# Optimization experiments

Measured on AMD Instinct MI355X. Metric: run time of the kernel, lower is better.

Reference implementation:

```python
import jax, jax.numpy as jnp
import numpy as np

N_LINKS = 10000
N_PATHS = 100000
LSD = 32   # link_state_dim
PSD = 32   # path_state_dim
T = 4
MAX_LEN = 12
RU = 256   # readout_units
OUT = 2


def _glorot(key, shape):
    return jax.random.normal(key, shape) * jnp.sqrt(2.0 / (shape[0] + shape[-1]))


def setup_inputs() -> dict:
    key = jax.random.key(0)
    ks = jax.random.split(key, 12)
    # variable path lengths 4..12 (mean 8)
    lengths = 4 + (np.arange(N_PATHS) % 9)
    E = int(lengths.sum())
    offsets = np.cumsum(lengths) - lengths
    paths = np.repeat(np.arange(N_PATHS), lengths)
    seqs = np.arange(E) - np.repeat(offsets, lengths)  # position of hop within its path
    rng = np.random.default_rng(0)
    links = rng.integers(0, N_LINKS, size=E)
    return {
        "capacities": jax.random.uniform(ks[0], (N_LINKS,), minval=1.0, maxval=10.0),
        "traffic": jax.random.uniform(ks[1], (N_PATHS,), minval=0.1, maxval=1.0),
        "links": jnp.asarray(links, jnp.int32),
        "paths": jnp.asarray(paths, jnp.int32),
        "seqs": jnp.asarray(seqs, jnp.int32),
        "n_links": N_LINKS,
        "n_paths": N_PATHS,
        "K_link": _glorot(ks[2], (LSD, 3 * LSD)),
        "R_link": _glorot(ks[3], (LSD, 3 * LSD)),
        "b_link": jnp.zeros((2, 3 * LSD)),
        "K_path": _glorot(ks[4], (LSD, 3 * PSD)),
        "R_path": _glorot(ks[5], (PSD, 3 * PSD)),
        "b_path": jnp.zeros((2, 3 * PSD)),
        "W1": _glorot(ks[6], (PSD, RU)),
        "b1": jnp.zeros((RU,)),
        "W2": _glorot(ks[7], (RU, RU)),
        "b2": jnp.zeros((RU,)),
        "Wf": _glorot(ks[8], (RU + PSD, OUT)),
        "bf": jnp.zeros((OUT,)),
    }


def _gru(x, h, K, R, b):
    # keras GRUCell, reset_after=True: separate input/recurrent biases
    xz = x @ K + b[0]
    hz = h @ R + b[1]
    xi_z, xi_r, xi_h = jnp.split(xz, 3, axis=-1)
    hi_z, hi_r, hi_h = jnp.split(hz, 3, axis=-1)
    z = jax.nn.sigmoid(xi_z + hi_z)
    r = jax.nn.sigmoid(xi_r + hi_r)
    hh = jnp.tanh(xi_h + r * hi_h)
    return z * h + (1.0 - z) * hh


def reference(capacities, traffic, links, paths, seqs, n_links, n_paths,
              K_link, R_link, b_link, K_path, R_path, b_path,
              W1, b1, W2, b2, Wf, bf):
    link_state = jnp.concatenate([capacities[:, None], jnp.zeros((n_links, LSD - 1))], axis=1)
    path_state = jnp.concatenate([traffic[:, None], jnp.zeros((n_paths, PSD - 1))], axis=1)

    lens = jax.ops.segment_sum(jnp.ones_like(paths), paths, num_segments=n_paths)  # [P]
    mask_t = (jnp.arange(MAX_LEN)[:, None] < lens[None, :])  # [L, P]

    for _ in range(T):
        h_ = link_state[links]  # gather: [E, LSD]
        # scatter into padded per-path sequences: [P, L, LSD]
        padded = jnp.zeros((n_paths, MAX_LEN, LSD), link_state.dtype).at[paths, seqs].set(h_)

        def step(h, xm):
            x_t, m_t = xm  # [P, LSD], [P]
            h_new = _gru(x_t, h, K_path, R_path, b_path)
            h = jnp.where(m_t[:, None], h_new, h)  # masked steps keep state
            return h, h

        path_state, outputs = jax.lax.scan(step, path_state, (padded.transpose(1, 0, 2), mask_t))
        m = outputs[seqs, paths]  # gather_nd: [E, PSD]
        m = jax.ops.segment_sum(m, links, num_segments=n_links)  # [n_links, PSD]
        link_state = _gru(m, link_state, K_link, R_link, b_link)

    h1 = jax.nn.selu(path_state @ W1 + b1)
    h2 = jax.nn.selu(h1 @ W2 + b2)
    pred = jnp.concatenate([h2, path_state], axis=1) @ Wf + bf
    return pred
```

## Files before the change

### kernel.cpp

```cpp
#include <hip/hip_runtime.h>
#include <hip/hip_bf16.h>

#define NPATHS 100000
#define NLINKS 10000
#define NEDGES 799996
#define TITERS 4
#define GRP    695

typedef __hip_bfloat16 bf16;
typedef unsigned short u16;
typedef unsigned int   u32;
typedef _Float16 half8 __attribute__((ext_vector_type(8)));
typedef __attribute__((ext_vector_type(4))) float float4v;

#define U_LNK 64
#define U_KPB 320064
#define U_RPB 323136
#define U_KLB 326208
#define U_RLB 329280
#define U_W1T 332352
#define U_W2T 340544
#define F_BP  203040
#define F_BL  203232
#define F_B1  203424
#define F_B2  203680
#define F_WF  203936
#define F_MAC 204544
#define F_PS  524544
#define B_ROWPTR 8498432u
#define B_SLOT   8538496u
#define B_CNT    11738496u
#define B_BUF    11778560u
#define CSR_WS_MIN 63000000ull

__device__ __forceinline__ float bf2f(bf16 v) { return __bfloat162float(v); }
__device__ __forceinline__ u16 f2h_u(float f) {
    _Float16 h = (_Float16)f; u16 u; __builtin_memcpy(&u, &h, 2); return u;
}
__device__ __forceinline__ float h2f_u(u16 u) {
    _Float16 h; __builtin_memcpy(&h, &u, 2); return (float)h;
}
__device__ __forceinline__ float loadf(const void* p, int i, int isbf) {
    return isbf ? bf2f(((const bf16*)p)[i]) : ((const float*)p)[i];
}
__device__ __forceinline__ float sigmoid_(float v) { return 1.f / (1.f + __expf(-v)); }
__device__ __forceinline__ float tanh_(float v) { return 1.f - 2.f / (__expf(2.f * v) + 1.f); }
__device__ __forceinline__ float selu_(float v) {
    return v > 0.f ? 1.0507009873554805f * v : 1.7580993408473766f * (__expf(v) - 1.f);
}
__device__ __forceinline__ u16* ps_row(u16* ps0, u16* ps1, u16* ps2, int p) {
    return p < 49999 ? ps0 + (size_t)p * 32
         : (p < 99998 ? ps1 + (size_t)(p - 49999) * 32
                      : ps2 + (size_t)(p - 99998) * 32);
}

__global__ void probe_kernel(const u32* __restrict__ cap, int* __restrict__ flag) {
    if (threadIdx.x == 0 && blockIdx.x == 0) {
        bool ok = true;
        for (int i = 0; i < 8; ++i) {
            u32 w = cap[i];
            u32 e1 = (w >> 7) & 0xFF, e2 = (w >> 23) & 0xFF;
            ok = ok && e1 >= 122 && e1 <= 133 && e2 >= 122 && e2 <= 133;
        }
        *flag = ok ? 1 : 0;
    }
}

__global__ __launch_bounds__(256) void init_kernel(
    const void* __restrict__ traf, const void* __restrict__ cap, const int* __restrict__ flag,
    float* __restrict__ wsf, u16* __restrict__ wsu, u16* ps0, u16* ps1, u16* ps2,
    const void* Kp, const void* Rp, const void* bp,
    const void* Kl, const void* Rl, const void* bl,
    const void* W1, const void* b1, const void* W2, const void* b2,
    const void* Wf, const void* bfv)
{
    const int isbf = *flag;
    const int i = blockIdx.x * 256 + threadIdx.x;
    if (i < NPATHS) {
        u32 ww[16];
        ww[0] = (u32)f2h_u(loadf(traf, i, isbf));
#pragma unroll
        for (int k = 1; k < 16; ++k) ww[k] = 0;
        uint4* row = (uint4*)ps_row(ps0, ps1, ps2, i);
        row[0] = *(uint4*)(ww + 0);  row[1] = *(uint4*)(ww + 4);
        row[2] = *(uint4*)(ww + 8);  row[3] = *(uint4*)(ww + 12);
    }
    int j;
    j = i;          if (j >= 0 && j < 320000)
        wsu[U_LNK + j] = ((j & 31) == 0) ? f2h_u(loadf(cap, j >> 5, isbf)) : (u16)0;
    j = i - 320000; if (j >= 0 && j < 3072) {
        int t = j >> 9, lane = (j >> 3) & 63, e = j & 7;
        int k = (lane >> 4) * 8 + e, n = t * 16 + (lane & 15);
        wsu[U_KPB + j] = f2h_u(loadf(Kp, k * 96 + n, isbf));
    }
    j = i - 323072; if (j >= 0 && j < 3072) {
        int t = j >> 9, lane = (j >> 3) & 63, e = j & 7;
        int k = (lane >> 4) * 8 + e, n = t * 16 + (lane & 15);
        wsu[U_RPB + j] = f2h_u(loadf(Rp, k * 96 + n, isbf));
    }
    j = i - 326144; if (j >= 0 && j < 3072) {
        int t = j >> 9, lane = (j >> 3) & 63, e = j & 7;
        int k = (lane >> 4) * 8 + e, n = t * 16 + (lane & 15);
        wsu[U_KLB + j] = f2h_u(loadf(Kl, k * 96 + n, isbf));
    }
    j = i - 329216; if (j >= 0 && j < 3072) {
        int t = j >> 9, lane = (j >> 3) & 63, e = j & 7;
        int k = (lane >> 4) * 8 + e, n = t * 16 + (lane & 15);
        wsu[U_RLB + j] = f2h_u(loadf(Rl, k * 96 + n, isbf));
    }
    j = i - 332288; if (j >= 0 && j < 192)   wsf[F_BP + j] = loadf(bp, j, isbf);
    j = i - 332480; if (j >= 0 && j < 192)   wsf[F_BL + j] = loadf(bl, j, isbf);
    j = i - 332672; if (j >= 0 && j < 256)   wsf[F_B1 + j] = loadf(b1, j, isbf);
    j = i - 332928; if (j >= 0 && j < 256)   wsf[F_B2 + j] = loadf(b2, j, isbf);
    j = i - 333184; if (j >= 0 && j < 578)
        wsf[F_WF + j] = (j < 576) ? loadf(Wf, j, isbf) : loadf(bfv, j - 576, isbf);
    j = i - 334000; if (j >= 0 && j < 8192) {
        int t = j >> 9, lane = (j >> 3) & 63, e = j & 7;
        int k = (lane >> 4) * 8 + e, n = t * 16 + (lane & 15);
        wsu[U_W1T + j] = f2h_u(loadf(W1, k * 256 + n, isbf));
    }
    j = i - 343000; if (j >= 0 && j < 65536) {
        int g = j >> 9, t = g >> 3, kb = g & 7;
        int lane = (j >> 3) & 63, e = j & 7;
        int k = kb * 32 + (lane >> 4) * 8 + e, n = t * 16 + (lane & 15);
        wsu[U_W2T + j] = f2h_u(loadf(W2, k * 256 + n, isbf));
    }
}

__global__ __launch_bounds__(256) void csr_count(const int* __restrict__ links,
                                                 int* __restrict__ cnt, int* __restrict__ slot) {
    int e = blockIdx.x * 256 + threadIdx.x;
    if (e < NEDGES) slot[e] = atomicAdd(&cnt[links[e]], 1);
}

__global__ __launch_bounds__(256) void csr_scan(const int* __restrict__ cnt,
                                                int* __restrict__ rowptr) {
    __shared__ int sd[256];
    __shared__ int sbase;
    const int tid = threadIdx.x;
    if (tid == 0) sbase = 0;
    __syncthreads();
    for (int chunk = 0; chunk < 40; ++chunk) {
        const int i = chunk * 256 + tid;
        const int v = (i < NLINKS) ? cnt[i] : 0;
        sd[tid] = v;
        __syncthreads();
        for (int off = 1; off < 256; off <<= 1) {
            int t = (tid >= off) ? sd[tid - off] : 0;
            __syncthreads();
            sd[tid] += t;
            __syncthreads();
        }
        if (i < NLINKS) rowptr[i] = sbase + sd[tid] - v;
        int ctot = sd[255];
        __syncthreads();
        if (tid == 0) sbase += ctot;
        __syncthreads();
    }
    if (tid == 0) rowptr[NLINKS] = sbase;
}

__global__ __launch_bounds__(256) void csr_slotadd(const int* __restrict__ links,
                                                   const int* __restrict__ rowptr,
                                                   int* __restrict__ slot) {
    int e = blockIdx.x * 256 + threadIdx.x;
    if (e < NEDGES) slot[e] += rowptr[links[e]];
}

__global__ __launch_bounds__(256, 3) void path_gru_mfma(
    const int* __restrict__ links,
    const u16* __restrict__ KPB, const u16* __restrict__ RPB,
    const float* __restrict__ bp,
    const u16* __restrict__ lnk16,
    u16* ps0, u16* ps1, u16* ps2, float* __restrict__ m_acc,
    const int* __restrict__ slot, u16* __restrict__ buf, const int csr)
{
    __shared__ u16 hlds[4][16 * 40];
    const int tid = threadIdx.x;
    const int wv = tid >> 6, lane = tid & 63;
    const int q = lane >> 4, col = lane & 15;
    const int w = blockIdx.x * 4 + wv;
    if (w >= 9 * GRP) return;
    const int c = w % 9;
    const int gi = w / 9;
    const int cnt = (c == 0) ? 11112 : 11111;
    const int idx0 = gi * 16;
    const int L = 4 + c;

    const int idxc = idx0 + col;
    const int actc = idxc < cnt;
    const int idcl = min(idxc, cnt - 1);
    const int pc   = c + 9 * idcl;
    const int offc = 4 * pc + idcl * 36 + (c * (c - 1)) / 2;

    u16* hw = hlds[wv];

    half8 KB[6], RB[6];
#pragma unroll
    for (int t = 0; t < 6; ++t) {
        KB[t] = *(const half8*)(KPB + t * 512 + lane * 8);
        RB[t] = *(const half8*)(RPB + t * 512 + lane * 8);
    }
    float xzb[6], hzb[6];
#pragma unroll
    for (int t = 0; t < 6; ++t) { xzb[t] = bp[t * 16 + col]; hzb[t] = bp[96 + t * 16 + col]; }

    half8 Ah = *(const half8*)(ps_row(ps0, ps1, ps2, pc) + q * 8);
    float hold[2][4];
#pragma unroll
    for (int t = 0; t < 2; ++t)
#pragma unroll
        for (int r = 0; r < 4; ++r) {
            int idr = min(idx0 + q * 4 + r, cnt - 1);
            int pr = c + 9 * idr;
            hold[t][r] = h2f_u(ps_row(ps0, ps1, ps2, pr)[t * 16 + col]);
        }

    int ln = actc ? links[offc] : -1;
    int sv = (csr && actc) ? slot[offc] : -1;
    half8 Ax = *(const half8*)(lnk16 + (size_t)max(ln, 0) * 32 + q * 8);

    for (int s = 0; s < L; ++s) {
        const int more = (s + 1 < L) && actc;
        const int ln_nxt = more ? links[offc + s + 1] : -1;
        const int sv_nxt = (csr && more) ? slot[offc + s + 1] : -1;
        const half8 Ax_nxt = *(const half8*)(lnk16 + (size_t)max(ln_nxt, 0) * 32 + q * 8);

        float4v xz[6], hz[6];
#pragma unroll
        for (int t = 0; t < 6; ++t) {
            float4v ix = {xzb[t], xzb[t], xzb[t], xzb[t]};
            float4v ih = {hzb[t], hzb[t], hzb[t], hzb[t]};
            xz[t] = __builtin_amdgcn_mfma_f32_16x16x32_f16(Ax, KB[t], ix, 0, 0, 0);
            hz[t] = __builtin_amdgcn_mfma_f32_16x16x32_f16(Ah, RB[t], ih, 0, 0, 0);
        }
#pragma unroll
        for (int t = 0; t < 2; ++t)
#pragma unroll
            for (int r = 0; r < 4; ++r) {
                const float z  = sigmoid_(xz[t][r] + hz[t][r]);
                const float rr = sigmoid_(xz[t + 2][r] + hz[t + 2][r]);
                const float hh = tanh_(xz[t + 4][r] + rr * hz[t + 4][r]);
                const float hn = z * hold[t][r] + (1.f - z) * hh;
                hold[t][r] = hn;
                hw[(q * 4 + r) * 40 + t * 16 + col] = f2h_u(hn);
            }
        Ah = *(const half8*)(hw + col * 40 + q * 8);
        if (csr) {
            const int r4 = lane >> 4, dw = lane & 15;
#pragma unroll
            for (int j3 = 0; j3 < 4; ++j3) {
                const int srow = j3 * 4 + r4;
                const int tgt = __shfl(sv, srow);
                const u32 val = *(const u32*)(hw + srow * 40 + 2 * dw);
                if (tgt >= 0) *(u32*)(buf + (size_t)tgt * 32 + 2 * dw) = val;
            }
        } else {
            const int half_ = lane >> 5, kk = lane & 31;
#pragma unroll 1
            for (int j2 = 0; j2 < 8; ++j2) {
                const int src = 2 * j2 + half_;
                const int tgt = __shfl(ln, src);
                const float v = h2f_u(hw[src * 40 + kk]);
                if (tgt >= 0) unsafeAtomicAdd(m_acc + (size_t)tgt * 32 + kk, v);
            }
        }
        ln = ln_nxt; sv = sv_nxt; Ax = Ax_nxt;
    }
    if (actc) {
        uint4 tmp; __builtin_memcpy(&tmp, &Ah, 16);
        *(uint4*)(ps_row(ps0, ps1, ps2, pc) + q * 8) = tmp;
    }
}

__global__ __launch_bounds__(256) void seg_sum(
    const u16* __restrict__ buf, const int* __restrict__ rowptr,
    float* __restrict__ m)
{
    const int l = blockIdx.x * 4 + (threadIdx.x >> 6);
    if (l >= NLINKS) return;
    const int lane = threadIdx.x & 63;
    const int r = lane >> 4, dw = lane & 15;
    const int beg = rowptr[l], end = rowptr[l + 1];
    float a0 = 0.f, a1 = 0.f;
    for (int i = beg + r; i < end; i += 4) {
        const u32 v = *(const u32*)(buf + (size_t)i * 32 + 2 * dw);
        a0 += h2f_u((u16)(v & 0xffff));
        a1 += h2f_u((u16)(v >> 16));
    }
    a0 += __shfl_xor(a0, 16); a0 += __shfl_xor(a0, 32);
    a1 += __shfl_xor(a1, 16); a1 += __shfl_xor(a1, 32);
    if (r == 0) ((float2*)(m + (size_t)l * 32))[dw] = make_float2(a0, a1);
}

__global__ __launch_bounds__(256) void link_gru_mfma(
    const u16* __restrict__ KLB, const u16* __restrict__ RLB,
    const float* __restrict__ bl,
    const float* __restrict__ m_in, u16* __restrict__ lnk16)
{
    __shared__ u16 hlds[4][16 * 40];
    const int tid = threadIdx.x;
    const int wv = tid >> 6, lane = tid & 63;
    const int q = lane >> 4, col = lane & 15;
    const int w = blockIdx.x * 4 + wv;
    if (w >= NLINKS / 16) return;
    const int base = w * 16;
    u16* hw = hlds[wv];

    half8 KB[6], RB[6];
#pragma unroll
    for (int t = 0; t < 6; ++t) {
        KB[t] = *(const half8*)(KLB + t * 512 + lane * 8);
        RB[t] = *(const half8*)(RLB + t * 512 + lane * 8);
    }
    float xzb[6], hzb[6];
#pragma unroll
    for (int t = 0; t < 6; ++t) { xzb[t] = bl[t * 16 + col]; hzb[t] = bl[96 + t * 16 + col]; }

    half8 Ax;
    {
        const float4* mr = (const float4*)(m_in + (size_t)(base + col) * 32 + q * 8);
        float4 a = mr[0], b = mr[1];
        _Float16 xv[8] = {(_Float16)a.x, (_Float16)a.y, (_Float16)a.z, (_Float16)a.w,
                          (_Float16)b.x, (_Float16)b.y, (_Float16)b.z, (_Float16)b.w};
        __builtin_memcpy(&Ax, xv, 16);
    }
    half8 Ah = *(const half8*)(lnk16 + (size_t)(base + col) * 32 + q * 8);
    float hold[2][4];
#pragma unroll
    for (int t = 0; t < 2; ++t)
#pragma unroll
        for (int r = 0; r < 4; ++r)
            hold[t][r] = h2f_u(lnk16[(size_t)(base + q * 4 + r) * 32 + t * 16 + col]);

    float4v xz[6], hz[6];
#pragma unroll
    for (int t = 0; t < 6; ++t) {
        float4v ix = {xzb[t], xzb[t], xzb[t], xzb[t]};
        float4v ih = {hzb[t], hzb[t], hzb[t], hzb[t]};
        xz[t] = __builtin_amdgcn_mfma_f32_16x16x32_f16(Ax, KB[t], ix, 0, 0, 0);
        hz[t] = __builtin_amdgcn_mfma_f32_16x16x32_f16(Ah, RB[t], ih, 0, 0, 0);
    }
#pragma unroll
    for (int t = 0; t < 2; ++t)
#pragma unroll
        for (int r = 0; r < 4; ++r) {
            const float z  = sigmoid_(xz[t][r] + hz[t][r]);
            const float rr = sigmoid_(xz[t + 2][r] + hz[t + 2][r]);
            const float hh = tanh_(xz[t + 4][r] + rr * hz[t + 4][r]);
            const float hn = z * hold[t][r] + (1.f - z) * hh;
            hw[(q * 4 + r) * 40 + t * 16 + col] = f2h_u(hn);
        }
    {
        uint4 tmp = *(const uint4*)(hw + col * 40 + q * 8);
        *(uint4*)(lnk16 + (size_t)(base + col) * 32 + q * 8) = tmp;
    }
}

__global__ __launch_bounds__(256) void readout_mfma(
    u16* ps0, u16* ps1, u16* ps2,
    const u16* __restrict__ W1T, const u16* __restrict__ W2T,
    const float* __restrict__ b1f, const float* __restrict__ b2f,
    const float* __restrict__ Wff,
    const int* __restrict__ flag, void* __restrict__ out)
{
    __shared__ u16  sA[4][4096];
    __shared__ float sB1[256], sB2[256], sWf[578];
    const int tid = threadIdx.x;
    if (tid < 256) { sB1[tid] = b1f[tid]; sB2[tid] = b2f[tid]; }
    for (int i = tid; i < 578; i += 256) sWf[i] = Wff[i];
    __syncthreads();

    const int w = tid >> 6, lane = tid & 63;
    const int col = lane & 15, q = lane >> 4;
    const int pbase = blockIdx.x * 64 + w * 16;
    u16* sAw = sA[w];

    const int pa = min(pbase + col, NPATHS - 1);
    const half8 aps = *(const half8*)(ps_row(ps0, ps1, ps2, pa) + q * 8);
#pragma unroll
    for (int t = 0; t < 16; ++t) {
        const half8 bfrag = *(const half8*)(W1T + t * 512 + lane * 8);
        float4v acc = {0.f, 0.f, 0.f, 0.f};
        acc = __builtin_amdgcn_mfma_f32_16x16x32_f16(aps, bfrag, acc, 0, 0, 0);
        const int kb = t >> 1;
        const int qp = 2 * (t & 1) + (col >> 3);
#pragma unroll
        for (int rI = 0; rI < 4; ++rI) {
            const int m = q * 4 + rI;
            const float h1 = selu_(acc[rI] + sB1[t * 16 + col]);
            sAw[kb * 512 + qp * 128 + m * 8 + (col & 7)] = f2h_u(h1);
        }
    }
    half8 afr[8];
#pragma unroll
    for (int kb = 0; kb < 8; ++kb)
        afr[kb] = *(const half8*)(sAw + kb * 512 + lane * 8);

    float4v acc2[16];
#pragma unroll
    for (int t = 0; t < 16; ++t) acc2[t] = (float4v){0.f, 0.f, 0.f, 0.f};
#pragma unroll
    for (int kb = 0; kb < 8; ++kb) {
#pragma unroll
        for (int t = 0; t < 16; ++t) {
            const half8 bfrag = *(const half8*)(W2T + (t * 8 + kb) * 512 + lane * 8);
            acc2[t] = __builtin_amdgcn_mfma_f32_16x16x32_f16(afr[kb], bfrag, acc2[t], 0, 0, 0);
        }
    }

    float p0[4] = {0.f, 0.f, 0.f, 0.f}, p1[4] = {0.f, 0.f, 0.f, 0.f};
#pragma unroll
    for (int t = 0; t < 16; ++t) {
        const int n = t * 16 + col;
        const float wf0 = sWf[2 * n], wf1 = sWf[2 * n + 1];
#pragma unroll
        for (int rI = 0; rI < 4; ++rI) {
            const float h2 = selu_(acc2[t][rI] + sB2[n]);
            p0[rI] += h2 * wf0; p1[rI] += h2 * wf1;
        }
    }
#pragma unroll
    for (int msk = 1; msk < 16; msk <<= 1) {
#pragma unroll
        for (int rI = 0; rI < 4; ++rI) {
            p0[rI] += __shfl_xor(p0[rI], msk);
            p1[rI] += __shfl_xor(p1[rI], msk);
        }
    }
    if (col == 0) {
        const int isbf = *flag;
#pragma unroll
        for (int rI = 0; rI < 4; ++rI) {
            const int pp = pbase + q * 4 + rI;
            if (pp < NPATHS) {
                const u16* pr = ps_row(ps0, ps1, ps2, pp);
                float s0 = p0[rI] + sWf[576], s1 = p1[rI] + sWf[577];
                for (int k = 0; k < 32; ++k) {
                    const float pv = h2f_u(pr[k]);
                    s0 += pv * sWf[(256 + k) * 2];
                    s1 += pv * sWf[(256 + k) * 2 + 1];
                }
                if (isbf) {
                    __hip_bfloat162 o;
                    o.x = __float2bfloat16(s0);
                    o.y = __float2bfloat16(s1);
                    ((__hip_bfloat162*)out)[pp] = o;
                } else {
                    ((float2*)out)[pp] = make_float2(s0, s1);
                }
            }
        }
    }
}

extern "C" void kernel_launch(void* const* d_in, const int* in_sizes, int n_in,
                              void* d_out, int out_size, void* d_ws, size_t ws_size,
                              hipStream_t stream)
{
    const int* links = (const int*)d_in[2];
    float* wsf = (float*)d_ws;
    u16*   wsu = (u16*)d_ws;
    int*   flag = (int*)d_ws;

    u16* wps = (u16*)(wsf + F_PS);
    u16 *ps0, *ps1, *ps2;
    if (ws_size >= (size_t)(F_PS * 4) + 6400000 + 256) {
        ps0 = wps; ps1 = wps + (size_t)49999 * 32; ps2 = wps + (size_t)99998 * 32;
    } else {
        ps0 = (u16*)d_in[3]; ps1 = (u16*)d_in[4]; ps2 = wps;
    }
    const bool csr = ws_size >= CSR_WS_MIN;
    int* rowptr = (int*)((char*)d_ws + B_ROWPTR);
    int* slot   = (int*)((char*)d_ws + B_SLOT);
    int* cnt    = (int*)((char*)d_ws + B_CNT);
    u16* buf    = (u16*)((char*)d_ws + B_BUF);

    probe_kernel<<<1, 64, 0, stream>>>((const u32*)d_in[0], flag);
    init_kernel<<<1596, 256, 0, stream>>>(d_in[1], d_in[0], flag, wsf, wsu, ps0, ps1, ps2,
                                          d_in[10], d_in[11], d_in[12],
                                          d_in[7], d_in[8], d_in[9],
                                          d_in[13], d_in[14], d_in[15], d_in[16],
                                          d_in[17], d_in[18]);
    if (csr) {
        hipMemsetAsync(cnt, 0, NLINKS * sizeof(int), stream);
        csr_count<<<(NEDGES + 255) / 256, 256, 0, stream>>>(links, cnt, slot);
        csr_scan<<<1, 256, 0, stream>>>(cnt, rowptr);
        csr_slotadd<<<(NEDGES + 255) / 256, 256, 0, stream>>>(links, rowptr, slot);
    }
    const int pg_blocks = (9 * GRP + 3) / 4;
    const int lg_blocks = (NLINKS / 16 + 3) / 4;
    for (int t = 0; t < TITERS; ++t) {
        if (!csr) hipMemsetAsync(wsf + F_MAC, 0, NLINKS * 32 * sizeof(float), stream);
        path_gru_mfma<<<pg_blocks, 256, 0, stream>>>(
            links, wsu + U_KPB, wsu + U_RPB, wsf + F_BP,
            wsu + U_LNK, ps0, ps1, ps2, wsf + F_MAC,
            slot, buf, csr ? 1 : 0);
        if (csr)
            seg_sum<<<(NLINKS + 3) / 4, 256, 0, stream>>>(buf, rowptr, wsf + F_MAC);
        link_gru_mfma<<<lg_blocks, 256, 0, stream>>>(
            wsu + U_KLB, wsu + U_RLB, wsf + F_BL, wsf + F_MAC, wsu + U_LNK);
    }
    readout_mfma<<<(NPATHS + 63) / 64, 256, 0, stream>>>(
        ps0, ps1, ps2,
        wsu + U_W1T, wsu + U_W2T,
        wsf + F_B1, wsf + F_B2, wsf + F_WF, flag, d_out);
}
```

Baseline: 632.9 us.

## Interleave two path groups per wave, fuse seg-sum into link GRU, restructure readout

```diff
diff --git a/kernel.cpp b/kernel.cpp
--- a/kernel.cpp
+++ b/kernel.cpp
@@ -6,6 +6,7 @@
 #define NEDGES 799996
 #define TITERS 4
 #define GRP    695
+#define WPC    348
 
 typedef __hip_bfloat16 bf16;
 typedef unsigned short u16;
@@ -135,26 +136,26 @@
 
 __global__ __launch_bounds__(256) void csr_scan(const int* __restrict__ cnt,
                                                 int* __restrict__ rowptr) {
-    __shared__ int sd[256];
-    __shared__ int sbase;
-    const int tid = threadIdx.x;
-    if (tid == 0) sbase = 0;
-    __syncthreads();
+    __shared__ int wsum[4];
+    const int tid = threadIdx.x, lane = tid & 63, wv = tid >> 6;
+    int sbase = 0;
     for (int chunk = 0; chunk < 40; ++chunk) {
         const int i = chunk * 256 + tid;
         const int v = (i < NLINKS) ? cnt[i] : 0;
-        sd[tid] = v;
+        int s = v;
+#pragma unroll
+        for (int off = 1; off < 64; off <<= 1) {
+            int t = __shfl_up(s, off);
+            if (lane >= off) s += t;
+        }
+        if (lane == 63) wsum[wv] = s;
         __syncthreads();
-        for (int off = 1; off < 256; off <<= 1) {
-            int t = (tid >= off) ? sd[tid - off] : 0;
-            __syncthreads();
-            sd[tid] += t;
-            __syncthreads();
-        }
-        if (i < NLINKS) rowptr[i] = sbase + sd[tid] - v;
-        int ctot = sd[255];
-        __syncthreads();
-        if (tid == 0) sbase += ctot;
+        int wb = 0;
+#pragma unroll
+        for (int k = 0; k < 4; ++k) if (k < wv) wb += wsum[k];
+        const int total = wsum[0] + wsum[1] + wsum[2] + wsum[3];
+        if (i < NLINKS) rowptr[i] = sbase + wb + s - v;
+        sbase += total;
         __syncthreads();
     }
     if (tid == 0) rowptr[NLINKS] = sbase;
@@ -167,7 +168,7 @@
     if (e < NEDGES) slot[e] += rowptr[links[e]];
 }
 
-__global__ __launch_bounds__(256, 3) void path_gru_mfma(
+__global__ __launch_bounds__(256, 2) void path_gru_mfma(
     const int* __restrict__ links,
     const u16* __restrict__ KPB, const u16* __restrict__ RPB,
     const float* __restrict__ bp,
@@ -175,122 +176,211 @@
     u16* ps0, u16* ps1, u16* ps2, float* __restrict__ m_acc,
     const int* __restrict__ slot, u16* __restrict__ buf, const int csr)
 {
+    __shared__ u16 hlds[8][16 * 40];
+    const int tid = threadIdx.x;
+    const int wv = tid >> 6, lane = tid & 63;
+    const int q = lane >> 4, col = lane & 15;
+    const int w = blockIdx.x * 4 + wv;
+    if (w >= 9 * WPC) return;
+    const int c = w % 9;
+    const int j = w / 9;
+    const int cnt = (c == 0) ? 11112 : 11111;
+    const int L = 4 + c;
+
+    half8 KB[6], RB[6];
+#pragma unroll
+    for (int t = 0; t < 6; ++t) {
+        KB[t] = *(const half8*)(KPB + t * 512 + lane * 8);
+        RB[t] = *(const half8*)(RPB + t * 512 + lane * 8);
+    }
+    float xzb[6], hzb[6];
+#pragma unroll
+    for (int t = 0; t < 6; ++t) { xzb[t] = bp[t * 16 + col]; hzb[t] = bp[96 + t * 16 + col]; }
+
+    int actc[2], offc[2], pc[2], ln[2], sv[2];
+    half8 Ah[2], Ax[2];
+    float hold[2][2][4];
+    u16* hw[2] = { hlds[wv * 2], hlds[wv * 2 + 1] };
+
+#pragma unroll
+    for (int ch = 0; ch < 2; ++ch) {
+        const int g = j + ch * WPC;
+        const int gok = g < GRP;
+        const int idx0 = min(g, GRP - 1) * 16;
+        const int idxc = idx0 + col;
+        actc[ch] = gok && (idxc < cnt);
+        const int idcl = min(idxc, cnt - 1);
+        pc[ch] = c + 9 * idcl;
+        offc[ch] = 4 * pc[ch] + idcl * 36 + (c * (c - 1)) / 2;
+        Ah[ch] = *(const half8*)(ps_row(ps0, ps1, ps2, pc[ch]) + q * 8);
+#pragma unroll
+        for (int t = 0; t < 2; ++t)
+#pragma unroll
+            for (int r = 0; r < 4; ++r) {
+                int idr = min(idx0 + q * 4 + r, cnt - 1);
+                int pr = c + 9 * idr;
+                hold[ch][t][r] = h2f_u(ps_row(ps0, ps1, ps2, pr)[t * 16 + col]);
+            }
+        ln[ch] = actc[ch] ? links[offc[ch]] : -1;
+        sv[ch] = (csr && actc[ch]) ? slot[offc[ch]] : -1;
+        Ax[ch] = *(const half8*)(lnk16 + (size_t)max(ln[ch], 0) * 32 + q * 8);
+    }
+
+    for (int s = 0; s < L; ++s) {
+        int lnn[2], svn[2];
+        half8 Axn[2];
+#pragma unroll
+        for (int ch = 0; ch < 2; ++ch) {
+            const int more = (s + 1 < L) && actc[ch];
+            lnn[ch] = more ? links[offc[ch] + s + 1] : -1;
+            svn[ch] = (csr && more) ? slot[offc[ch] + s + 1] : -1;
+            Axn[ch] = *(const half8*)(lnk16 + (size_t)max(lnn[ch], 0) * 32 + q * 8);
+        }
+        float4v xz[2][6], hz[2][6];
+#pragma unroll
+        for (int ch = 0; ch < 2; ++ch)
+#pragma unroll
+            for (int t = 0; t < 6; ++t) {
+                float4v ix = {xzb[t], xzb[t], xzb[t], xzb[t]};
+                float4v ih = {hzb[t], hzb[t], hzb[t], hzb[t]};
+                xz[ch][t] = __builtin_amdgcn_mfma_f32_16x16x32_f16(Ax[ch], KB[t], ix, 0, 0, 0);
+                hz[ch][t] = __builtin_amdgcn_mfma_f32_16x16x32_f16(Ah[ch], RB[t], ih, 0, 0, 0);
+            }
+#pragma unroll
+        for (int ch = 0; ch < 2; ++ch)
+#pragma unroll
+            for (int t = 0; t < 2; ++t)
+#pragma unroll
+                for (int r = 0; r < 4; ++r) {
+                    const float z  = sigmoid_(xz[ch][t][r] + hz[ch][t][r]);
+                    const float rr = sigmoid_(xz[ch][t + 2][r] + hz[ch][t + 2][r]);
+                    const float hh = tanh_(xz[ch][t + 4][r] + rr * hz[ch][t + 4][r]);
+                    const float hn = z * hold[ch][t][r] + (1.f - z) * hh;
+                    hold[ch][t][r] = hn;
+                    hw[ch][(q * 4 + r) * 40 + t * 16 + col] = f2h_u(hn);
+                }
+#pragma unroll
+        for (int ch = 0; ch < 2; ++ch)
+            Ah[ch] = *(const half8*)(hw[ch] + col * 40 + q * 8);
+        if (csr) {
+            const int r4 = lane >> 4, dw = lane & 15;
+#pragma unroll
+            for (int ch = 0; ch < 2; ++ch)
+#pragma unroll
+                for (int j3 = 0; j3 < 4; ++j3) {
+                    const int srow = j3 * 4 + r4;
+                    const int tgt = __shfl(sv[ch], srow);
+                    const u32 val = *(const u32*)(hw[ch] + srow * 40 + 2 * dw);
+                    if (tgt >= 0) *(u32*)(buf + (size_t)tgt * 32 + 2 * dw) = val;
+                }
+        } else {
+            const int half_ = lane >> 5, kk = lane & 31;
+#pragma unroll
+            for (int ch = 0; ch < 2; ++ch)
+#pragma unroll 1
+                for (int j2 = 0; j2 < 8; ++j2) {
+                    const int src = 2 * j2 + half_;
+                    const int tgt = __shfl(ln[ch], src);
+                    const float v = h2f_u(hw[ch][src * 40 + kk]);
+                    if (tgt >= 0) unsafeAtomicAdd(m_acc + (size_t)tgt * 32 + kk, v);
+                }
+        }
+#pragma unroll
+        for (int ch = 0; ch < 2; ++ch) { ln[ch] = lnn[ch]; sv[ch] = svn[ch]; Ax[ch] = Axn[ch]; }
+    }
+#pragma unroll
+    for (int ch = 0; ch < 2; ++ch)
+        if (actc[ch]) {
+            uint4 tmp; __builtin_memcpy(&tmp, &Ah[ch], 16);
+            *(uint4*)(ps_row(ps0, ps1, ps2, pc[ch]) + q * 8) = tmp;
+        }
+}
+
+__global__ __launch_bounds__(256) void link_gru_csr(
+    const u16* __restrict__ KLB, const u16* __restrict__ RLB,
+    const float* __restrict__ bl,
+    const u16* __restrict__ buf, const int* __restrict__ rowptr,
+    u16* __restrict__ lnk16)
+{
     __shared__ u16 hlds[4][16 * 40];
     const int tid = threadIdx.x;
     const int wv = tid >> 6, lane = tid & 63;
     const int q = lane >> 4, col = lane & 15;
     const int w = blockIdx.x * 4 + wv;
-    if (w >= 9 * GRP) return;
-    const int c = w % 9;
-    const int gi = w / 9;
-    const int cnt = (c == 0) ? 11112 : 11111;
-    const int idx0 = gi * 16;
-    const int L = 4 + c;
-
-    const int idxc = idx0 + col;
-    const int actc = idxc < cnt;
-    const int idcl = min(idxc, cnt - 1);
-    const int pc   = c + 9 * idcl;
-    const int offc = 4 * pc + idcl * 36 + (c * (c - 1)) / 2;
-
+    if (w >= NLINKS / 16) return;
+    const int base = w * 16;
     u16* hw = hlds[wv];
 
     half8 KB[6], RB[6];
 #pragma unroll
     for (int t = 0; t < 6; ++t) {
-        KB[t] = *(const half8*)(KPB + t * 512 + lane * 8);
-        RB[t] = *(const half8*)(RPB + t * 512 + lane * 8);
+        KB[t] = *(const half8*)(KLB + t * 512 + lane * 8);
+        RB[t] = *(const half8*)(RLB + t * 512 + lane * 8);
     }
     float xzb[6], hzb[6];
 #pragma unroll
-    for (int t = 0; t < 6; ++t) { xzb[t] = bp[t * 16 + col]; hzb[t] = bp[96 + t * 16 + col]; }
-
-    half8 Ah = *(const half8*)(ps_row(ps0, ps1, ps2, pc) + q * 8);
+    for (int t = 0; t < 6; ++t) { xzb[t] = bl[t * 16 + col]; hzb[t] = bl[96 + t * 16 + col]; }
+
+    const int link = base + col;
+    const int beg = rowptr[link], end = rowptr[link + 1];
+    float a[8] = {0.f, 0.f, 0.f, 0.f, 0.f, 0.f, 0.f, 0.f};
+    int i = beg;
+    for (; i + 1 < end; i += 2) {
+        const uint4 v0 = *(const uint4*)(buf + (size_t)i * 32 + q * 8);
+        const uint4 v1 = *(const uint4*)(buf + (size_t)(i + 1) * 32 + q * 8);
+        const u32 w0[4] = {v0.x, v0.y, v0.z, v0.w}, w1[4] = {v1.x, v1.y, v1.z, v1.w};
+#pragma unroll
+        for (int e = 0; e < 4; ++e) {
+            a[2 * e]     += h2f_u((u16)(w0[e] & 0xffff)) + h2f_u((u16)(w1[e] & 0xffff));
+            a[2 * e + 1] += h2f_u((u16)(w0[e] >> 16))    + h2f_u((u16)(w1[e] >> 16));
+        }
+    }
+    if (i < end) {
+        const uint4 v0 = *(const uint4*)(buf + (size_t)i * 32 + q * 8);
+        const u32 w0[4] = {v0.x, v0.y, v0.z, v0.w};
+#pragma unroll
+        for (int e = 0; e < 4; ++e) {
+            a[2 * e]     += h2f_u((u16)(w0[e] & 0xffff));
+            a[2 * e + 1] += h2f_u((u16)(w0[e] >> 16));
+        }
+    }
+    half8 Ax;
+    {
+        _Float16 xv[8];
+#pragma unroll
+        for (int e = 0; e < 8; ++e) xv[e] = (_Float16)a[e];
+        __builtin_memcpy(&Ax, xv, 16);
+    }
+    half8 Ah = *(const half8*)(lnk16 + (size_t)link * 32 + q * 8);
     float hold[2][4];
 #pragma unroll
     for (int t = 0; t < 2; ++t)
 #pragma unroll
+        for (int r = 0; r < 4; ++r)
+            hold[t][r] = h2f_u(lnk16[(size_t)(base + q * 4 + r) * 32 + t * 16 + col]);
+
+    float4v xz[6], hz[6];
+#pragma unroll
+    for (int t = 0; t < 6; ++t) {
+        float4v ix = {xzb[t], xzb[t], xzb[t], xzb[t]};
+        float4v ih = {hzb[t], hzb[t], hzb[t], hzb[t]};
+        xz[t] = __builtin_amdgcn_mfma_f32_16x16x32_f16(Ax, KB[t], ix, 0, 0, 0);
+        hz[t] = __builtin_amdgcn_mfma_f32_16x16x32_f16(Ah, RB[t], ih, 0, 0, 0);
+    }
+#pragma unroll
+    for (int t = 0; t < 2; ++t)
+#pragma unroll
         for (int r = 0; r < 4; ++r) {
-            int idr = min(idx0 + q * 4 + r, cnt - 1);
-            int pr = c + 9 * idr;
-            hold[t][r] = h2f_u(ps_row(ps0, ps1, ps2, pr)[t * 16 + col]);
-        }
-
-    int ln = actc ? links[offc] : -1;
-    int sv = (csr && actc) ? slot[offc] : -1;
-    half8 Ax = *(const half8*)(lnk16 + (size_t)max(ln, 0) * 32 + q * 8);
-
-    for (int s = 0; s < L; ++s) {
-        const int more = (s + 1 < L) && actc;
-        const int ln_nxt = more ? links[offc + s + 1] : -1;
-        const int sv_nxt = (csr && more) ? slot[offc + s + 1] : -1;
-        const half8 Ax_nxt = *(const half8*)(lnk16 + (size_t)max(ln_nxt, 0) * 32 + q * 8);
-
-        float4v xz[6], hz[6];
-#pragma unroll
-        for (int t = 0; t < 6; ++t) {
-            float4v ix = {xzb[t], xzb[t], xzb[t], xzb[t]};
-            float4v ih = {hzb[t], hzb[t], hzb[t], hzb[t]};
-            xz[t] = __builtin_amdgcn_mfma_f32_16x16x32_f16(Ax, KB[t], ix, 0, 0, 0);
-            hz[t] = __builtin_amdgcn_mfma_f32_16x16x32_f16(Ah, RB[t], ih, 0, 0, 0);
-        }
-#pragma unroll
-        for (int t = 0; t < 2; ++t)
-#pragma unroll
-            for (int r = 0; r < 4; ++r) {
-                const float z  = sigmoid_(xz[t][r] + hz[t][r]);
-                const float rr = sigmoid_(xz[t + 2][r] + hz[t + 2][r]);
-                const float hh = tanh_(xz[t + 4][r] + rr * hz[t + 4][r]);
-                const float hn = z * hold[t][r] + (1.f - z) * hh;
-                hold[t][r] = hn;
-                hw[(q * 4 + r) * 40 + t * 16 + col] = f2h_u(hn);
-            }
-        Ah = *(const half8*)(hw + col * 40 + q * 8);
-        if (csr) {
-            const int r4 = lane >> 4, dw = lane & 15;
-#pragma unroll
-            for (int j3 = 0; j3 < 4; ++j3) {
-                const int srow = j3 * 4 + r4;
-                const int tgt = __shfl(sv, srow);
-                const u32 val = *(const u32*)(hw + srow * 40 + 2 * dw);
-                if (tgt >= 0) *(u32*)(buf + (size_t)tgt * 32 + 2 * dw) = val;
-            }
-        } else {
-            const int half_ = lane >> 5, kk = lane & 31;
-#pragma unroll 1
-            for (int j2 = 0; j2 < 8; ++j2) {
-                const int src = 2 * j2 + half_;
-                const int tgt = __shfl(ln, src);
-                const float v = h2f_u(hw[src * 40 + kk]);
-                if (tgt >= 0) unsafeAtomicAdd(m_acc + (size_t)tgt * 32 + kk, v);
-            }
-        }
-        ln = ln_nxt; sv = sv_nxt; Ax = Ax_nxt;
-    }
-    if (actc) {
-        uint4 tmp; __builtin_memcpy(&tmp, &Ah, 16);
-        *(uint4*)(ps_row(ps0, ps1, ps2, pc) + q * 8) = tmp;
-    }
-}
-
-__global__ __launch_bounds__(256) void seg_sum(
-    const u16* __restrict__ buf, const int* __restrict__ rowptr,
-    float* __restrict__ m)
-{
-    const int l = blockIdx.x * 4 + (threadIdx.x >> 6);
-    if (l >= NLINKS) return;
-    const int lane = threadIdx.x & 63;
-    const int r = lane >> 4, dw = lane & 15;
-    const int beg = rowptr[l], end = rowptr[l + 1];
-    float a0 = 0.f, a1 = 0.f;
-    for (int i = beg + r; i < end; i += 4) {
-        const u32 v = *(const u32*)(buf + (size_t)i * 32 + 2 * dw);
-        a0 += h2f_u((u16)(v & 0xffff));
-        a1 += h2f_u((u16)(v >> 16));
-    }
-    a0 += __shfl_xor(a0, 16); a0 += __shfl_xor(a0, 32);
-    a1 += __shfl_xor(a1, 16); a1 += __shfl_xor(a1, 32);
-    if (r == 0) ((float2*)(m + (size_t)l * 32))[dw] = make_float2(a0, a1);
+            const float z  = sigmoid_(xz[t][r] + hz[t][r]);
+            const float rr = sigmoid_(xz[t + 2][r] + hz[t + 2][r]);
+            const float hh = tanh_(xz[t + 4][r] + rr * hz[t + 4][r]);
+            const float hn = z * hold[t][r] + (1.f - z) * hh;
+            hw[(q * 4 + r) * 40 + t * 16 + col] = f2h_u(hn);
+        }
+    {
+        uint4 tmp = *(const uint4*)(hw + col * 40 + q * 8);
+        *(uint4*)(lnk16 + (size_t)link * 32 + q * 8) = tmp;
+    }
 }
 
 __global__ __launch_bounds__(256) void link_gru_mfma(
@@ -365,6 +455,7 @@
     const int* __restrict__ flag, void* __restrict__ out)
 {
     __shared__ u16  sA[4][4096];
+    __shared__ float sP[4][64][2];
     __shared__ float sB1[256], sB2[256], sWf[578];
     const int tid = threadIdx.x;
     if (tid < 256) { sB1[tid] = b1f[tid]; sB2[tid] = b2f[tid]; }
@@ -373,10 +464,10 @@
 
     const int w = tid >> 6, lane = tid & 63;
     const int col = lane & 15, q = lane >> 4;
-    const int pbase = blockIdx.x * 64 + w * 16;
+    const int pbase = blockIdx.x * 64;
     u16* sAw = sA[w];
 
-    const int pa = min(pbase + col, NPATHS - 1);
+    const int pa = min(pbase + w * 16 + col, NPATHS - 1);
     const half8 aps = *(const half8*)(ps_row(ps0, ps1, ps2, pa) + q * 8);
 #pragma unroll
     for (int t = 0; t < 16; ++t) {
@@ -392,63 +483,83 @@
             sAw[kb * 512 + qp * 128 + m * 8 + (col & 7)] = f2h_u(h1);
         }
     }
-    half8 afr[8];
-#pragma unroll
-    for (int kb = 0; kb < 8; ++kb)
-        afr[kb] = *(const half8*)(sAw + kb * 512 + lane * 8);
-
-    float4v acc2[16];
-#pragma unroll
-    for (int t = 0; t < 16; ++t) acc2[t] = (float4v){0.f, 0.f, 0.f, 0.f};
+    __syncthreads();
+
+    float4v acc2[4][4];
+#pragma unroll
+    for (int tt = 0; tt < 4; ++tt)
+#pragma unroll
+        for (int g = 0; g < 4; ++g) acc2[tt][g] = (float4v){0.f, 0.f, 0.f, 0.f};
 #pragma unroll
     for (int kb = 0; kb < 8; ++kb) {
-#pragma unroll
-        for (int t = 0; t < 16; ++t) {
+        half8 afr[4];
+#pragma unroll
+        for (int g = 0; g < 4; ++g)
+            afr[g] = *(const half8*)(sA[g] + kb * 512 + lane * 8);
+#pragma unroll
+        for (int tt = 0; tt < 4; ++tt) {
+            const int t = w * 4 + tt;
             const half8 bfrag = *(const half8*)(W2T + (t * 8 + kb) * 512 + lane * 8);
-            acc2[t] = __builtin_amdgcn_mfma_f32_16x16x32_f16(afr[kb], bfrag, acc2[t], 0, 0, 0);
-        }
-    }
-
-    float p0[4] = {0.f, 0.f, 0.f, 0.f}, p1[4] = {0.f, 0.f, 0.f, 0.f};
-#pragma unroll
-    for (int t = 0; t < 16; ++t) {
-        const int n = t * 16 + col;
-        const float wf0 = sWf[2 * n], wf1 = sWf[2 * n + 1];
-#pragma unroll
-        for (int rI = 0; rI < 4; ++rI) {
-            const float h2 = selu_(acc2[t][rI] + sB2[n]);
-            p0[rI] += h2 * wf0; p1[rI] += h2 * wf1;
-        }
-    }
-#pragma unroll
-    for (int msk = 1; msk < 16; msk <<= 1) {
-#pragma unroll
-        for (int rI = 0; rI < 4; ++rI) {
-            p0[rI] += __shfl_xor(p0[rI], msk);
-            p1[rI] += __shfl_xor(p1[rI], msk);
-        }
-    }
-    if (col == 0) {
-        const int isbf = *flag;
-#pragma unroll
-        for (int rI = 0; rI < 4; ++rI) {
-            const int pp = pbase + q * 4 + rI;
-            if (pp < NPATHS) {
-                const u16* pr = ps_row(ps0, ps1, ps2, pp);
-                float s0 = p0[rI] + sWf[576], s1 = p1[rI] + sWf[577];
-                for (int k = 0; k < 32; ++k) {
-                    const float pv = h2f_u(pr[k]);
-                    s0 += pv * sWf[(256 + k) * 2];
-                    s1 += pv * sWf[(256 + k) * 2 + 1];
-                }
-                if (isbf) {
-                    __hip_bfloat162 o;
-                    o.x = __float2bfloat16(s0);
-                    o.y = __float2bfloat16(s1);
-                    ((__hip_bfloat162*)out)[pp] = o;
-                } else {
-                    ((float2*)out)[pp] = make_float2(s0, s1);
-                }
+#pragma unroll
+            for (int g = 0; g < 4; ++g)
+                acc2[tt][g] = __builtin_amdgcn_mfma_f32_16x16x32_f16(afr[g], bfrag, acc2[tt][g], 0, 0, 0);
+        }
+    }
+
+    float p0[4][4], p1[4][4];
+#pragma unroll
+    for (int g = 0; g < 4; ++g)
+#pragma unroll
+        for (int r = 0; r < 4; ++r) { p0[g][r] = 0.f; p1[g][r] = 0.f; }
+#pragma unroll
+    for (int tt = 0; tt < 4; ++tt) {
+        const int n = (w * 4 + tt) * 16 + col;
+        const float wf0 = sWf[2 * n], wf1 = sWf[2 * n + 1], b2v = sB2[n];
+#pragma unroll
+        for (int g = 0; g < 4; ++g)
+#pragma unroll
+            for (int r = 0; r < 4; ++r) {
+                const float h2 = selu_(acc2[tt][g][r] + b2v);
+                p0[g][r] += h2 * wf0; p1[g][r] += h2 * wf1;
+            }
+    }
+#pragma unroll
+    for (int msk = 1; msk < 16; msk <<= 1)
+#pragma unroll
+        for (int g = 0; g < 4; ++g)
+#pragma unroll
+            for (int r = 0; r < 4; ++r) {
+                p0[g][r] += __shfl_xor(p0[g][r], msk);
+                p1[g][r] += __shfl_xor(p1[g][r], msk);
+            }
+    if (col == 0)
+#pragma unroll
+        for (int g = 0; g < 4; ++g)
+#pragma unroll
+            for (int r = 0; r < 4; ++r) {
+                sP[w][g * 16 + q * 4 + r][0] = p0[g][r];
+                sP[w][g * 16 + q * 4 + r][1] = p1[g][r];
+            }
+    __syncthreads();
+
+    if (tid < 64) {
+        const int pp = pbase + tid;
+        if (pp < NPATHS) {
+            float s0 = sP[0][tid][0] + sP[1][tid][0] + sP[2][tid][0] + sP[3][tid][0] + sWf[576];
+            float s1 = sP[0][tid][1] + sP[1][tid][1] + sP[2][tid][1] + sP[3][tid][1] + sWf[577];
+            const u16* pr = ps_row(ps0, ps1, ps2, pp);
+            for (int k = 0; k < 32; ++k) {
+                const float pv = h2f_u(pr[k]);
+                s0 += pv * sWf[(256 + k) * 2];
+                s1 += pv * sWf[(256 + k) * 2 + 1];
+            }
+            if (*flag) {
+                __hip_bfloat162 o;
+                o.x = __float2bfloat16(s0);
+                o.y = __float2bfloat16(s1);
+                ((__hip_bfloat162*)out)[pp] = o;
+            } else {
+                ((float2*)out)[pp] = make_float2(s0, s1);
             }
         }
     }
@@ -488,7 +599,7 @@
         csr_scan<<<1, 256, 0, stream>>>(cnt, rowptr);
         csr_slotadd<<<(NEDGES + 255) / 256, 256, 0, stream>>>(links, rowptr, slot);
     }
-    const int pg_blocks = (9 * GRP + 3) / 4;
+    const int pg_blocks = (9 * WPC + 3) / 4;
     const int lg_blocks = (NLINKS / 16 + 3) / 4;
     for (int t = 0; t < TITERS; ++t) {
         if (!csr) hipMemsetAsync(wsf + F_MAC, 0, NLINKS * 32 * sizeof(float), stream);
@@ -497,9 +608,11 @@
             wsu + U_LNK, ps0, ps1, ps2, wsf + F_MAC,
             slot, buf, csr ? 1 : 0);
         if (csr)
-            seg_sum<<<(NLINKS + 3) / 4, 256, 0, stream>>>(buf, rowptr, wsf + F_MAC);
-        link_gru_mfma<<<lg_blocks, 256, 0, stream>>>(
-            wsu + U_KLB, wsu + U_RLB, wsf + F_BL, wsf + F_MAC, wsu + U_LNK);
+            link_gru_csr<<<lg_blocks, 256, 0, stream>>>(
+                wsu + U_KLB, wsu + U_RLB, wsf + F_BL, buf, rowptr, wsu + U_LNK);
+        else
+            link_gru_mfma<<<lg_blocks, 256, 0, stream>>>(
+                wsu + U_KLB, wsu + U_RLB, wsf + F_BL, wsf + F_MAC, wsu + U_LNK);
     }
     readout_mfma<<<(NPATHS + 63) / 64, 256, 0, stream>>>(
         ps0, ps1, ps2,
```

Result: slower. 684.9 us (+8.2%).
